# Kernel tuning notes

Measured on AMD Instinct MI355X. Metric: run time of the kernel, lower is better.

Reference implementation:

```python
import jax, jax.numpy as jnp
import numpy as np


def conv3d(x, w, b):
    # x: (B,C,T,W,H), w: (O,I,3,3,3), 'same' padding, stride 1
    y = jax.lax.conv_general_dilated(x, w, (1, 1, 1), [(1, 1)] * 3,
                                     dimension_numbers=('NCDHW', 'OIDHW', 'NCDHW'))
    return y + b[None, :, None, None, None]


def mamba(x, W_in, W_conv, b_conv, W_xproj, W_dt, b_dt, A_log, D, W_out):
    # x: (b, L, d_model) -> (b, L, d_model). Standard Mamba block.
    d_inner, d_state = A_log.shape
    d_conv = W_conv.shape[-1]
    dt_rank = W_dt.shape[1]
    xz = x @ W_in.T                                   # (b, L, 2*d_inner)
    xs, z = jnp.split(xz, 2, axis=-1)
    # causal depthwise conv1d (torch pads d_conv-1 both sides then truncates to L)
    xc = jnp.transpose(xs, (0, 2, 1))                 # (b, d_inner, L)
    xc = jax.lax.conv_general_dilated(xc, W_conv, (1,), [(d_conv - 1, 0)],
                                      feature_group_count=d_inner,
                                      dimension_numbers=('NCH', 'OIH', 'NCH'))
    xc = xc + b_conv[None, :, None]
    xc = jax.nn.silu(jnp.transpose(xc, (0, 2, 1)))    # (b, L, d_inner)
    x_dbl = xc @ W_xproj.T                            # (b, L, dt_rank + 2*d_state)
    dt, B, C = jnp.split(x_dbl, [dt_rank, dt_rank + d_state], axis=-1)
    dt = jax.nn.softplus(dt @ W_dt.T + b_dt)          # (b, L, d_inner)
    A = -jnp.exp(A_log)                               # (d_inner, d_state)
    deltaA = jnp.exp(dt[..., None] * A)               # (b, L, d_inner, d_state)
    deltaBx = dt[..., None] * B[:, :, None, :] * xc[..., None]

    def comb(c1, c2):
        a1, b1 = c1
        a2, b2 = c2
        return a1 * a2, a2 * b1 + b2

    _, hs = jax.lax.associative_scan(comb, (deltaA, deltaBx), axis=1)
    y = jnp.einsum('blds,bls->bld', hs, C) + xc * D   # (b, L, d_inner)
    y = y * jax.nn.silu(z)
    return y @ W_out.T                                # (b, L, d_model)


def setup_inputs() -> dict:
    key = jax.random.key(0)
    ks = jax.random.split(key, 12)
    b, c, t, w, h = 2, 3, 8, 96, 96
    d_state, d_conv, expand = 16, 4, 2
    d_inner = expand * c           # 6
    dt_rank = max(1, -(-c // 16))  # ceil(c/16) = 1

    def n(k, shape, s=0.02):
        return jax.random.normal(k, shape, jnp.float32) * s

    return {
        'x': jax.random.normal(ks[0], (b, c, t, w, h), jnp.float32),
        'W_cb1': n(ks[1], (16, c, 3, 3, 3)), 'b_cb1': jnp.zeros(16, jnp.float32),
        'W_cb2': n(ks[2], (c, 16, 3, 3, 3)), 'b_cb2': jnp.zeros(c, jnp.float32),
        'W_in': n(ks[3], (2 * d_inner, c)),
        'W_conv': n(ks[4], (d_inner, 1, d_conv), 0.2), 'b_conv': jnp.zeros(d_inner, jnp.float32),
        'W_xproj': n(ks[5], (dt_rank + 2 * d_state, d_inner), 0.1),
        'W_dt': n(ks[6], (d_inner, dt_rank), 0.5), 'b_dt': n(ks[7], (d_inner,), 0.1),
        'A_log': jnp.log(jnp.tile(jnp.arange(1, d_state + 1, dtype=jnp.float32)[None, :], (d_inner, 1))),
        'D': jnp.ones(d_inner, jnp.float32),
        'W_out': n(ks[8], (c, d_inner)),
        'W_sm': n(ks[9], (c, c, 3, 3, 3)), 'b_sm': jnp.zeros(c, jnp.float32),
    }


def reference(x, W_cb1, b_cb1, W_cb2, b_cb2, W_in, W_conv, b_conv, W_xproj,
              W_dt, b_dt, A_log, D, W_out, W_sm, b_sm):
    b, c, t, w, h = x.shape
    xr = conv3d(jax.nn.relu(conv3d(x, W_cb1, b_cb1)), W_cb2, b_cb2) + x
    # faithful to torch: x.reshape(b, -1, c) on contiguous (b,c,t,w,h)
    xs = xr.reshape(b, t * w * h, c)
    y = mamba(xs, W_in, W_conv, b_conv, W_xproj, W_dt, b_dt, A_log, D, W_out)
    y = jnp.transpose(y, (0, 2, 1)).reshape(b, c, t, w, h)
    return conv3d(y, W_sm, b_sm)
```

## Files before the change

### kernel.cpp

```cpp
#include <hip/hip_runtime.h>
#include <math.h>

#define L_      73728
#define CTHW_   221184
#define CH_     128
#define NCK_    576
#define STRD_   132
#define LOG2E_  1.4426950408889634f

#define PZS_    9604
#define PCS_    96040
#define XPAD_N  576240
#define T1P_N   3073280
#define YMP_N   576240
#define ZERO_N  (XPAD_N + T1P_N + YMP_N + 16)

__device__ __forceinline__ float silu_(float x) {
    return x / (1.f + __expf(-x));
}
__device__ __forceinline__ float softplus_(float x) {
    return (x > 20.f) ? x : log1pf(__expf(x));
}

__global__ __launch_bounds__(256) void k0_zero(float4* __restrict__ p, int n4) {
    int i = blockIdx.x * 256 + threadIdx.x;
    if (i < n4) p[i] = make_float4(0.f, 0.f, 0.f, 0.f);
}

__global__ __launch_bounds__(256) void k0_copy(const float* __restrict__ x,
        float* __restrict__ xpad) {
    int idx = blockIdx.x * 256 + threadIdx.x;
    int xx = idx % 96, yy = (idx / 96) % 96, z = (idx / 9216) % 8, bc = idx / 73728;
    xpad[bc * PCS_ + (z + 1) * PZS_ + (yy + 1) * 98 + (xx + 1)] = x[idx];
}

__global__ __launch_bounds__(256) void k1_conv(const float* __restrict__ xpad,
        const float* __restrict__ W, const float* __restrict__ b,
        float* __restrict__ t1p) {
    __shared__ float ws[81][16];
    __shared__ float bs[16];
    int tid = threadIdx.x;
    for (int i = tid; i < 1296; i += 256) ws[i % 81][i / 81] = W[i];
    if (tid < 16) bs[tid] = b[tid];
    __syncthreads();
    int idx = blockIdx.x * 256 + tid;
    int xx = idx % 96, yy = (idx / 96) % 96, tz = (idx / 9216) % 8, bb = idx / 73728;
    float acc[16];
    #pragma unroll
    for (int o = 0; o < 16; ++o) acc[o] = bs[o];
    int pbase = (tz + 1) * PZS_ + (yy + 1) * 98 + (xx + 1);
    #pragma unroll
    for (int ic = 0; ic < 3; ++ic) {
        const float* xp = xpad + (bb * 3 + ic) * PCS_ + pbase;
        float v[27];
        #pragma unroll
        for (int kz = 0; kz < 3; ++kz)
            #pragma unroll
            for (int ky = 0; ky < 3; ++ky)
                #pragma unroll
                for (int kx = 0; kx < 3; ++kx)
                    v[kz * 9 + ky * 3 + kx] = xp[(kz - 1) * PZS_ + (ky - 1) * 98 + (kx - 1)];
        #pragma unroll
        for (int k = 0; k < 27; ++k)
            #pragma unroll
            for (int o = 0; o < 16; ++o)
                acc[o] = fmaf(ws[ic * 27 + k][o], v[k], acc[o]);
    }
    float* op = t1p + bb * 16 * PCS_ + pbase;
    #pragma unroll
    for (int o = 0; o < 16; ++o) op[o * PCS_] = fmaxf(acc[o], 0.f);
}

__global__ __launch_bounds__(256) void k2_conv(const float* __restrict__ t1p,
        const float* __restrict__ W, const float* __restrict__ b,
        const float* __restrict__ x, float* __restrict__ xr) {
    __shared__ float ws[432][3];
    __shared__ float bs[3];
    int tid = threadIdx.x;
    for (int i = tid; i < 1296; i += 256) ws[i % 432][i / 432] = W[i];
    if (tid < 3) bs[tid] = b[tid];
    __syncthreads();
    int idx = blockIdx.x * 256 + tid;
    int xx = idx % 96, yy = (idx / 96) % 96, tz = (idx / 9216) % 8, bb = idx / 73728;
    float acc[3];
    #pragma unroll
    for (int o = 0; o < 3; ++o) acc[o] = bs[o];
    int pbase = (tz + 1) * PZS_ + (yy + 1) * 98 + (xx + 1);
    #pragma unroll 2
    for (int ic = 0; ic < 16; ++ic) {
        const float* xp = t1p + (bb * 16 + ic) * PCS_ + pbase;
        float v[27];
        #pragma unroll
        for (int kz = 0; kz < 3; ++kz)
            #pragma unroll
            for (int ky = 0; ky < 3; ++ky)
                #pragma unroll
                for (int kx = 0; kx < 3; ++kx)
                    v[kz * 9 + ky * 3 + kx] = xp[(kz - 1) * PZS_ + (ky - 1) * 98 + (kx - 1)];
        #pragma unroll
        for (int k = 0; k < 27; ++k)
            #pragma unroll
            for (int o = 0; o < 3; ++o)
                acc[o] = fmaf(ws[ic * 27 + k][o], v[k], acc[o]);
    }
    int sp = tz * 9216 + yy * 96 + xx;
    #pragma unroll
    for (int o = 0; o < 3; ++o) {
        int gi = (bb * 3 + o) * 73728 + sp;
        xr[gi] = acc[o] + x[gi];
    }
}

__global__ __launch_bounds__(128) void k4_carry(const float* __restrict__ xr,
        const float* __restrict__ W_in, const float* __restrict__ W_conv,
        const float* __restrict__ b_conv, const float* __restrict__ W_xproj,
        const float* __restrict__ W_dt, const float* __restrict__ b_dt,
        const float* __restrict__ A_log, float2* __restrict__ carries) {
    __shared__ float sf[28 * STRD_];
    __shared__ float s_Win[18], s_Wc[24], s_bc[6], s_Wx[102], s_Wdt[6], s_bdt[6];
    int tid = threadIdx.x;
    if (tid < 18) s_Win[tid] = W_in[tid];
    if (tid < 24) s_Wc[tid] = W_conv[tid];
    if (tid >= 32 && tid < 38) s_bc[tid - 32] = b_conv[tid - 32];
    if (tid >= 40 && tid < 46) { s_Wdt[tid - 40] = W_dt[tid - 40]; s_bdt[tid - 40] = b_dt[tid - 40]; }
    if (tid >= 64 && tid < 128) {
        for (int i = tid - 64; i < 102; i += 64) s_Wx[i] = W_xproj[i];
    }
    __syncthreads();
    int blk = blockIdx.x, b = blk / NCK_, ck = blk % NCK_;
    int l = ck * CH_ + tid;
    const float* xb = xr + b * CTHW_;
    float xin[4][6];
    #pragma unroll
    for (int k = 0; k < 4; ++k) {
        int r = l - 3 + k;
        float a0 = 0.f, a1 = 0.f, a2v = 0.f;
        if (r >= 0) { a0 = xb[3 * r]; a1 = xb[3 * r + 1]; a2v = xb[3 * r + 2]; }
        #pragma unroll
        for (int d = 0; d < 6; ++d)
            xin[k][d] = s_Win[d * 3] * a0 + s_Win[d * 3 + 1] * a1 + s_Win[d * 3 + 2] * a2v;
    }
    float xc[6];
    #pragma unroll
    for (int d = 0; d < 6; ++d) {
        float p = s_bc[d];
        #pragma unroll
        for (int k = 0; k < 4; ++k) p = fmaf(s_Wc[d * 4 + k], xin[k][d], p);
        xc[d] = silu_(p);
    }
    float dtraw = 0.f;
    #pragma unroll
    for (int d = 0; d < 6; ++d) dtraw = fmaf(s_Wx[d], xc[d], dtraw);
    #pragma unroll
    for (int d = 0; d < 6; ++d) {
        sf[(0 + d) * STRD_ + tid] = xc[d];
        sf[(6 + d) * STRD_ + tid] = softplus_(fmaf(dtraw, s_Wdt[d], s_bdt[d]));
    }
    #pragma unroll
    for (int s = 0; s < 16; ++s) {
        float pb = 0.f;
        #pragma unroll
        for (int d = 0; d < 6; ++d) pb = fmaf(s_Wx[(1 + s) * 6 + d], xc[d], pb);
        sf[(12 + s) * STRD_ + tid] = pb;
    }
    __syncthreads();
    if (tid < 96) {
        int d = tid >> 4, s = tid & 15;
        float a2 = -__expf(A_log[tid]) * LOG2E_;
        float h = 0.f, sdt = 0.f;
        #pragma unroll 8
        for (int i = 0; i < CH_; ++i) {
            float dt = sf[(6 + d) * STRD_ + i];
            float xcv = sf[d * STRD_ + i];
            float Bv = sf[(12 + s) * STRD_ + i];
            h = fmaf(exp2f(dt * a2), h, dt * xcv * Bv);
            sdt += dt;
        }
        carries[(b * 96 + tid) * NCK_ + ck] = make_float2(exp2f(sdt * a2), h);
    }
}

__global__ __launch_bounds__(576) void k5_scan(const float2* __restrict__ carries,
        float* __restrict__ hpref) {
    __shared__ float2 s0[NCK_], s1[NCK_];
    int t = threadIdx.x;
    int blk = blockIdx.x, b = blk / 96, r = blk % 96;
    s0[t] = carries[(b * 96 + r) * NCK_ + t];
    __syncthreads();
    float2* cur = s0;
    float2* nxt = s1;
    for (int off = 1; off < NCK_; off <<= 1) {
        float2 v = cur[t];
        if (t >= off) {
            float2 p = cur[t - off];
            v = make_float2(p.x * v.x, v.x * p.y + v.y);
        }
        nxt[t] = v;
        __syncthreads();
        float2* tmp = cur; cur = nxt; nxt = tmp;
    }
    float hp = (t == 0) ? 0.f : cur[t - 1].y;
    hpref[(b * NCK_ + t) * 96 + r] = hp;
}

__global__ __launch_bounds__(128) void k6_apply(const float* __restrict__ xr,
        const float* __restrict__ W_in, const float* __restrict__ W_conv,
        const float* __restrict__ b_conv, const float* __restrict__ W_xproj,
        const float* __restrict__ W_dt, const float* __restrict__ b_dt,
        const float* __restrict__ A_log, const float* __restrict__ Dp,
        const float* __restrict__ W_out, const float* __restrict__ hpref,
        float* __restrict__ ymp) {
    __shared__ float sf[50 * STRD_];
    __shared__ float ys[CH_ * 6];
    __shared__ float s_Win[36], s_Wc[24], s_bc[6], s_Wx[198], s_Wdt[6], s_bdt[6], s_wout[18];
    int tid = threadIdx.x;
    if (tid < 36) s_Win[tid] = W_in[tid];
    if (tid < 24) s_Wc[tid] = W_conv[tid];
    if (tid >= 36 && tid < 42) s_bc[tid - 36] = b_conv[tid - 36];
    if (tid >= 42 && tid < 48) { s_Wdt[tid - 42] = W_dt[tid - 42]; s_bdt[tid - 42] = b_dt[tid - 42]; }
    if (tid >= 48 && tid < 66) s_wout[tid - 48] = W_out[tid - 48];
    if (tid >= 64 && tid < 128) {
        for (int i = tid - 64; i < 198; i += 64) s_Wx[i] = W_xproj[i];
    }
    __syncthreads();
    int blk = blockIdx.x, b = blk / NCK_, ck = blk % NCK_;
    int l = ck * CH_ + tid;
    const float* xb = xr + b * CTHW_;
    float xin[4][6];
    float zv[6];
    #pragma unroll
    for (int k = 0; k < 4; ++k) {
        int r = l - 3 + k;
        float a0 = 0.f, a1 = 0.f, a2v = 0.f;
        if (r >= 0) { a0 = xb[3 * r]; a1 = xb[3 * r + 1]; a2v = xb[3 * r + 2]; }
        #pragma unroll
        for (int d = 0; d < 6; ++d)
            xin[k][d] = s_Win[d * 3] * a0 + s_Win[d * 3 + 1] * a1 + s_Win[d * 3 + 2] * a2v;
        if (k == 3) {
            #pragma unroll
            for (int d = 0; d < 6; ++d)
                zv[d] = s_Win[(6 + d) * 3] * a0 + s_Win[(6 + d) * 3 + 1] * a1 + s_Win[(6 + d) * 3 + 2] * a2v;
        }
    }
    float xc[6];
    #pragma unroll
    for (int d = 0; d < 6; ++d) {
        float p = s_bc[d];
        #pragma unroll
        for (int k = 0; k < 4; ++k) p = fmaf(s_Wc[d * 4 + k], xin[k][d], p);
        xc[d] = silu_(p);
    }
    float dtraw = 0.f;
    #pragma unroll
    for (int d = 0; d < 6; ++d) dtraw = fmaf(s_Wx[d], xc[d], dtraw);
    #pragma unroll
    for (int d = 0; d < 6; ++d) {
        sf[(0 + d) * STRD_ + tid] = xc[d];
        sf[(6 + d) * STRD_ + tid] = softplus_(fmaf(dtraw, s_Wdt[d], s_bdt[d]));
        sf[(12 + d) * STRD_ + tid] = zv[d];
    }
    #pragma unroll
    for (int s = 0; s < 16; ++s) {
        float pb = 0.f, pc = 0.f;
        #pragma unroll
        for (int d = 0; d < 6; ++d) {
            pb = fmaf(s_Wx[(1 + s) * 6 + d], xc[d], pb);
            pc = fmaf(s_Wx[(17 + s) * 6 + d], xc[d], pc);
        }
        sf[(18 + s) * STRD_ + tid] = pb;
        sf[(34 + s) * STRD_ + tid] = pc;
    }
    __syncthreads();
    if (tid < 96) {
        int d = tid >> 4, s = tid & 15;
        float a2 = -__expf(A_log[tid]) * LOG2E_;
        float Dd = Dp[d];
        float h = hpref[(b * NCK_ + ck) * 96 + tid];
        #pragma unroll 4
        for (int i0 = 0; i0 < CH_; i0 += 8) {
            float pb[8], xv[8];
            #pragma unroll
            for (int j = 0; j < 8; ++j) {
                int i = i0 + j;
                float dt = sf[(6 + d) * STRD_ + i];
                float xcv = sf[d * STRD_ + i];
                float Bv = sf[(18 + s) * STRD_ + i];
                float Cv = sf[(34 + s) * STRD_ + i];
                h = fmaf(exp2f(dt * a2), h, dt * xcv * Bv);
                pb[j] = h * Cv;
                xv[j] = xcv;
            }
            #pragma unroll
            for (int j = 0; j < 8; ++j) pb[j] += __shfl_xor(pb[j], 1, 16);
            #pragma unroll
            for (int j = 0; j < 8; ++j) pb[j] += __shfl_xor(pb[j], 2, 16);
            #pragma unroll
            for (int j = 0; j < 8; ++j) pb[j] += __shfl_xor(pb[j], 4, 16);
            #pragma unroll
            for (int j = 0; j < 8; ++j) pb[j] += __shfl_xor(pb[j], 8, 16);
            if (s == 0) {
                #pragma unroll
                for (int j = 0; j < 8; ++j) {
                    float zz = sf[(12 + d) * STRD_ + i0 + j];
                    ys[(i0 + j) * 6 + d] = fmaf(xv[j], Dd, pb[j]) * silu_(zz);
                }
            }
        }
    }
    __syncthreads();
    {
        float y0 = ys[tid * 6 + 0], y1 = ys[tid * 6 + 1], y2 = ys[tid * 6 + 2];
        float y3 = ys[tid * 6 + 3], y4 = ys[tid * 6 + 4], y5 = ys[tid * 6 + 5];
        int xx = l % 96, yy = (l / 96) % 96, tz = l / 9216;
        int pdst = (tz + 1) * PZS_ + (yy + 1) * 98 + (xx + 1);
        #pragma unroll
        for (int i = 0; i < 3; ++i) {
            float o = s_wout[i * 6 + 0] * y0 + s_wout[i * 6 + 1] * y1
                    + s_wout[i * 6 + 2] * y2 + s_wout[i * 6 + 3] * y3
                    + s_wout[i * 6 + 4] * y4 + s_wout[i * 6 + 5] * y5;
            ymp[(b * 3 + i) * PCS_ + pdst] = o;
        }
    }
}

__global__ __launch_bounds__(256) void k7_conv(const float* __restrict__ ymp,
        const float* __restrict__ W, const float* __restrict__ b,
        float* __restrict__ out) {
    __shared__ float ws[81][3];
    __shared__ float bs[3];
    int tid = threadIdx.x;
    for (int i = tid; i < 243; i += 256) ws[i % 81][i / 81] = W[i];
    if (tid < 3) bs[tid] = b[tid];
    __syncthreads();
    int idx = blockIdx.x * 256 + tid;
    int xx = idx % 96, yy = (idx / 96) % 96, tz = (idx / 9216) % 8, bb = idx / 73728;
    float acc[3];
    #pragma unroll
    for (int o = 0; o < 3; ++o) acc[o] = bs[o];
    int pbase = (tz + 1) * PZS_ + (yy + 1) * 98 + (xx + 1);
    #pragma unroll
    for (int ic = 0; ic < 3; ++ic) {
        const float* xp = ymp + (bb * 3 + ic) * PCS_ + pbase;
        float v[27];
        #pragma unroll
        for (int kz = 0; kz < 3; ++kz)
            #pragma unroll
            for (int ky = 0; ky < 3; ++ky)
                #pragma unroll
                for (int kx = 0; kx < 3; ++kx)
                    v[kz * 9 + ky * 3 + kx] = xp[(kz - 1) * PZS_ + (ky - 1) * 98 + (kx - 1)];
        #pragma unroll
        for (int k = 0; k < 27; ++k)
            #pragma unroll
            for (int o = 0; o < 3; ++o)
                acc[o] = fmaf(ws[ic * 27 + k][o], v[k], acc[o]);
    }
    int sp = tz * 9216 + yy * 96 + xx;
    #pragma unroll
    for (int o = 0; o < 3; ++o) out[(bb * 3 + o) * 73728 + sp] = acc[o];
}

extern "C" void kernel_launch(void* const* d_in, const int* in_sizes, int n_in,
                              void* d_out, int out_size, void* d_ws, size_t ws_size,
                              hipStream_t stream) {
    const float* x      = (const float*)d_in[0];
    const float* W_cb1  = (const float*)d_in[1];
    const float* b_cb1  = (const float*)d_in[2];
    const float* W_cb2  = (const float*)d_in[3];
    const float* b_cb2  = (const float*)d_in[4];
    const float* W_in   = (const float*)d_in[5];
    const float* W_conv = (const float*)d_in[6];
    const float* b_conv = (const float*)d_in[7];
    const float* W_xpr  = (const float*)d_in[8];
    const float* W_dt   = (const float*)d_in[9];
    const float* b_dt   = (const float*)d_in[10];
    const float* A_log  = (const float*)d_in[11];
    const float* Dp     = (const float*)d_in[12];
    const float* W_out  = (const float*)d_in[13];
    const float* W_sm   = (const float*)d_in[14];
    const float* b_sm   = (const float*)d_in[15];

    float* ws    = (float*)d_ws;
    float* xpad  = ws;
    float* t1p   = xpad + XPAD_N;
    float* ymp   = t1p + T1P_N;
    float* xr    = ws + ZERO_N;
    float2* carr = (float2*)(xr + 442368);
    float* hpref = xr + 442368 + 221184;
    float* out   = (float*)d_out;

    int n4 = ZERO_N / 4;
    k0_zero<<<(n4 + 255) / 256, 256, 0, stream>>>((float4*)ws, n4);
    k0_copy<<<1728, 256, 0, stream>>>(x, xpad);
    k1_conv<<<576, 256, 0, stream>>>(xpad, W_cb1, b_cb1, t1p);
    k2_conv<<<576, 256, 0, stream>>>(t1p, W_cb2, b_cb2, x, xr);
    k4_carry<<<1152, 128, 0, stream>>>(xr, W_in, W_conv, b_conv, W_xpr, W_dt, b_dt, A_log, carr);
    k5_scan<<<192, 576, 0, stream>>>(carr, hpref);
    k6_apply<<<1152, 128, 0, stream>>>(xr, W_in, W_conv, b_conv, W_xpr, W_dt, b_dt,
                                       A_log, Dp, W_out, hpref, ymp);
    k7_conv<<<576, 256, 0, stream>>>(ymp, W_sm, b_sm, out);
}
```

Before: 195.3 us.

## Register-block conv kernels over 4 outputs and halve scan chunk length

The two 3-output conv kernels now compute four adjacent x-outputs per thread, loading a 6-wide row per kernel row so input loads are reused across outputs. This cuts launched blocks from 576 to 144. The Mamba scan chunk shrinks from 128 to 64 positions, doubling the number of chunks and blocks. k5_scan pre-combines pairs of carries so it can keep 576 threads, then expands the prefix back to per-chunk states. The goal is shorter serial recurrence loops in k4 and k6 at the cost of half-idle threads in the per-position phases, more carry traffic, and fewer blocks for the conv kernels.

After: 214.5 us. 1.1x slower.

```diff
diff --git a/kernel.cpp b/kernel.cpp
--- a/kernel.cpp
+++ b/kernel.cpp
@@ -3,9 +3,9 @@
 
 #define L_      73728
 #define CTHW_   221184
-#define CH_     128
-#define NCK_    576
-#define STRD_   132
+#define CH_     64
+#define NCK_    1152
+#define STRD_   68
 #define LOG2E_  1.4426950408889634f
 
 #define PZS_    9604
@@ -81,34 +81,50 @@
     if (tid < 3) bs[tid] = b[tid];
     __syncthreads();
     int idx = blockIdx.x * 256 + tid;
-    int xx = idx % 96, yy = (idx / 96) % 96, tz = (idx / 9216) % 8, bb = idx / 73728;
-    float acc[3];
-    #pragma unroll
-    for (int o = 0; o < 3; ++o) acc[o] = bs[o];
-    int pbase = (tz + 1) * PZS_ + (yy + 1) * 98 + (xx + 1);
+    int xg = idx % 24, yy = (idx / 24) % 96, tz = (idx / 2304) % 8, bb = idx / 18432;
+    int x0 = xg * 4;
+    float acc[3][4];
+    #pragma unroll
+    for (int o = 0; o < 3; ++o)
+        #pragma unroll
+        for (int u = 0; u < 4; ++u) acc[o][u] = bs[o];
+    int pbase = (tz + 1) * PZS_ + (yy + 1) * 98 + (x0 + 1);
     #pragma unroll 2
     for (int ic = 0; ic < 16; ++ic) {
         const float* xp = t1p + (bb * 16 + ic) * PCS_ + pbase;
-        float v[27];
+        float v[9][6];
         #pragma unroll
         for (int kz = 0; kz < 3; ++kz)
             #pragma unroll
             for (int ky = 0; ky < 3; ++ky)
                 #pragma unroll
-                for (int kx = 0; kx < 3; ++kx)
-                    v[kz * 9 + ky * 3 + kx] = xp[(kz - 1) * PZS_ + (ky - 1) * 98 + (kx - 1)];
-        #pragma unroll
-        for (int k = 0; k < 27; ++k)
-            #pragma unroll
-            for (int o = 0; o < 3; ++o)
-                acc[o] = fmaf(ws[ic * 27 + k][o], v[k], acc[o]);
-    }
-    int sp = tz * 9216 + yy * 96 + xx;
-    #pragma unroll
-    for (int o = 0; o < 3; ++o) {
-        int gi = (bb * 3 + o) * 73728 + sp;
-        xr[gi] = acc[o] + x[gi];
-    }
+                for (int j = 0; j < 6; ++j)
+                    v[kz * 3 + ky][j] = xp[(kz - 1) * PZS_ + (ky - 1) * 98 + (j - 1)];
+        #pragma unroll
+        for (int kz = 0; kz < 3; ++kz)
+            #pragma unroll
+            for (int ky = 0; ky < 3; ++ky)
+                #pragma unroll
+                for (int kx = 0; kx < 3; ++kx) {
+                    int k = ic * 27 + kz * 9 + ky * 3 + kx;
+                    float w0 = ws[k][0], w1 = ws[k][1], w2 = ws[k][2];
+                    #pragma unroll
+                    for (int u = 0; u < 4; ++u) {
+                        float vv = v[kz * 3 + ky][kx + u];
+                        acc[0][u] = fmaf(w0, vv, acc[0][u]);
+                        acc[1][u] = fmaf(w1, vv, acc[1][u]);
+                        acc[2][u] = fmaf(w2, vv, acc[2][u]);
+                    }
+                }
+    }
+    int sp = tz * 9216 + yy * 96 + x0;
+    #pragma unroll
+    for (int o = 0; o < 3; ++o)
+        #pragma unroll
+        for (int u = 0; u < 4; ++u) {
+            int gi = (bb * 3 + o) * 73728 + sp + u;
+            xr[gi] = acc[o][u] + x[gi];
+        }
 }
 
 __global__ __launch_bounds__(128) void k4_carry(const float* __restrict__ xr,
@@ -128,40 +144,42 @@
     }
     __syncthreads();
     int blk = blockIdx.x, b = blk / NCK_, ck = blk % NCK_;
-    int l = ck * CH_ + tid;
-    const float* xb = xr + b * CTHW_;
-    float xin[4][6];
-    #pragma unroll
-    for (int k = 0; k < 4; ++k) {
-        int r = l - 3 + k;
-        float a0 = 0.f, a1 = 0.f, a2v = 0.f;
-        if (r >= 0) { a0 = xb[3 * r]; a1 = xb[3 * r + 1]; a2v = xb[3 * r + 2]; }
-        #pragma unroll
-        for (int d = 0; d < 6; ++d)
-            xin[k][d] = s_Win[d * 3] * a0 + s_Win[d * 3 + 1] * a1 + s_Win[d * 3 + 2] * a2v;
-    }
-    float xc[6];
-    #pragma unroll
-    for (int d = 0; d < 6; ++d) {
-        float p = s_bc[d];
-        #pragma unroll
-        for (int k = 0; k < 4; ++k) p = fmaf(s_Wc[d * 4 + k], xin[k][d], p);
-        xc[d] = silu_(p);
-    }
-    float dtraw = 0.f;
-    #pragma unroll
-    for (int d = 0; d < 6; ++d) dtraw = fmaf(s_Wx[d], xc[d], dtraw);
-    #pragma unroll
-    for (int d = 0; d < 6; ++d) {
-        sf[(0 + d) * STRD_ + tid] = xc[d];
-        sf[(6 + d) * STRD_ + tid] = softplus_(fmaf(dtraw, s_Wdt[d], s_bdt[d]));
-    }
-    #pragma unroll
-    for (int s = 0; s < 16; ++s) {
-        float pb = 0.f;
-        #pragma unroll
-        for (int d = 0; d < 6; ++d) pb = fmaf(s_Wx[(1 + s) * 6 + d], xc[d], pb);
-        sf[(12 + s) * STRD_ + tid] = pb;
+    if (tid < CH_) {
+        int l = ck * CH_ + tid;
+        const float* xb = xr + b * CTHW_;
+        float xin[4][6];
+        #pragma unroll
+        for (int k = 0; k < 4; ++k) {
+            int r = l - 3 + k;
+            float a0 = 0.f, a1 = 0.f, a2v = 0.f;
+            if (r >= 0) { a0 = xb[3 * r]; a1 = xb[3 * r + 1]; a2v = xb[3 * r + 2]; }
+            #pragma unroll
+            for (int d = 0; d < 6; ++d)
+                xin[k][d] = s_Win[d * 3] * a0 + s_Win[d * 3 + 1] * a1 + s_Win[d * 3 + 2] * a2v;
+        }
+        float xc[6];
+        #pragma unroll
+        for (int d = 0; d < 6; ++d) {
+            float p = s_bc[d];
+            #pragma unroll
+            for (int k = 0; k < 4; ++k) p = fmaf(s_Wc[d * 4 + k], xin[k][d], p);
+            xc[d] = silu_(p);
+        }
+        float dtraw = 0.f;
+        #pragma unroll
+        for (int d = 0; d < 6; ++d) dtraw = fmaf(s_Wx[d], xc[d], dtraw);
+        #pragma unroll
+        for (int d = 0; d < 6; ++d) {
+            sf[(0 + d) * STRD_ + tid] = xc[d];
+            sf[(6 + d) * STRD_ + tid] = softplus_(fmaf(dtraw, s_Wdt[d], s_bdt[d]));
+        }
+        #pragma unroll
+        for (int s = 0; s < 16; ++s) {
+            float pb = 0.f;
+            #pragma unroll
+            for (int d = 0; d < 6; ++d) pb = fmaf(s_Wx[(1 + s) * 6 + d], xc[d], pb);
+            sf[(12 + s) * STRD_ + tid] = pb;
+        }
     }
     __syncthreads();
     if (tid < 96) {
@@ -176,20 +194,23 @@
             h = fmaf(exp2f(dt * a2), h, dt * xcv * Bv);
             sdt += dt;
         }
-        carries[(b * 96 + tid) * NCK_ + ck] = make_float2(exp2f(sdt * a2), h);
+        carries[(size_t)(b * 96 + tid) * NCK_ + ck] = make_float2(exp2f(sdt * a2), h);
     }
 }
 
 __global__ __launch_bounds__(576) void k5_scan(const float2* __restrict__ carries,
         float* __restrict__ hpref) {
-    __shared__ float2 s0[NCK_], s1[NCK_];
+    __shared__ float2 s0[576], s1[576];
     int t = threadIdx.x;
     int blk = blockIdx.x, b = blk / 96, r = blk % 96;
-    s0[t] = carries[(b * 96 + r) * NCK_ + t];
+    const float4* cp = (const float4*)(carries + (size_t)(b * 96 + r) * NCK_);
+    float4 cc = cp[t];
+    float2 c0 = make_float2(cc.x, cc.y);
+    s0[t] = make_float2(cc.x * cc.z, cc.z * cc.y + cc.w);
     __syncthreads();
     float2* cur = s0;
     float2* nxt = s1;
-    for (int off = 1; off < NCK_; off <<= 1) {
+    for (int off = 1; off < 576; off <<= 1) {
         float2 v = cur[t];
         if (t >= off) {
             float2 p = cur[t - off];
@@ -199,8 +220,9 @@
         __syncthreads();
         float2* tmp = cur; cur = nxt; nxt = tmp;
     }
-    float hp = (t == 0) ? 0.f : cur[t - 1].y;
-    hpref[(b * NCK_ + t) * 96 + r] = hp;
+    float Ey = (t == 0) ? 0.f : cur[t - 1].y;
+    hpref[(size_t)(b * NCK_ + 2 * t) * 96 + r] = Ey;
+    hpref[(size_t)(b * NCK_ + 2 * t + 1) * 96 + r] = fmaf(c0.x, Ey, c0.y);
 }
 
 __global__ __launch_bounds__(128) void k6_apply(const float* __restrict__ xr,
@@ -211,7 +233,7 @@
         const float* __restrict__ W_out, const float* __restrict__ hpref,
         float* __restrict__ ymp) {
     __shared__ float sf[50 * STRD_];
-    __shared__ float ys[CH_ * 6];
+    __shared__ float ys[CH_ * 7];
     __shared__ float s_Win[36], s_Wc[24], s_bc[6], s_Wx[198], s_Wdt[6], s_bdt[6], s_wout[18];
     int tid = threadIdx.x;
     if (tid < 36) s_Win[tid] = W_in[tid];
@@ -224,59 +246,61 @@
     }
     __syncthreads();
     int blk = blockIdx.x, b = blk / NCK_, ck = blk % NCK_;
-    int l = ck * CH_ + tid;
-    const float* xb = xr + b * CTHW_;
-    float xin[4][6];
-    float zv[6];
-    #pragma unroll
-    for (int k = 0; k < 4; ++k) {
-        int r = l - 3 + k;
-        float a0 = 0.f, a1 = 0.f, a2v = 0.f;
-        if (r >= 0) { a0 = xb[3 * r]; a1 = xb[3 * r + 1]; a2v = xb[3 * r + 2]; }
-        #pragma unroll
-        for (int d = 0; d < 6; ++d)
-            xin[k][d] = s_Win[d * 3] * a0 + s_Win[d * 3 + 1] * a1 + s_Win[d * 3 + 2] * a2v;
-        if (k == 3) {
+    int l = ck * CH_ + (tid & (CH_ - 1));
+    if (tid < CH_) {
+        const float* xb = xr + b * CTHW_;
+        float xin[4][6];
+        float zv[6];
+        #pragma unroll
+        for (int k = 0; k < 4; ++k) {
+            int r = l - 3 + k;
+            float a0 = 0.f, a1 = 0.f, a2v = 0.f;
+            if (r >= 0) { a0 = xb[3 * r]; a1 = xb[3 * r + 1]; a2v = xb[3 * r + 2]; }
             #pragma unroll
             for (int d = 0; d < 6; ++d)
-                zv[d] = s_Win[(6 + d) * 3] * a0 + s_Win[(6 + d) * 3 + 1] * a1 + s_Win[(6 + d) * 3 + 2] * a2v;
-        }
-    }
-    float xc[6];
-    #pragma unroll
-    for (int d = 0; d < 6; ++d) {
-        float p = s_bc[d];
-        #pragma unroll
-        for (int k = 0; k < 4; ++k) p = fmaf(s_Wc[d * 4 + k], xin[k][d], p);
-        xc[d] = silu_(p);
-    }
-    float dtraw = 0.f;
-    #pragma unroll
-    for (int d = 0; d < 6; ++d) dtraw = fmaf(s_Wx[d], xc[d], dtraw);
-    #pragma unroll
-    for (int d = 0; d < 6; ++d) {
-        sf[(0 + d) * STRD_ + tid] = xc[d];
-        sf[(6 + d) * STRD_ + tid] = softplus_(fmaf(dtraw, s_Wdt[d], s_bdt[d]));
-        sf[(12 + d) * STRD_ + tid] = zv[d];
-    }
-    #pragma unroll
-    for (int s = 0; s < 16; ++s) {
-        float pb = 0.f, pc = 0.f;
+                xin[k][d] = s_Win[d * 3] * a0 + s_Win[d * 3 + 1] * a1 + s_Win[d * 3 + 2] * a2v;
+            if (k == 3) {
+                #pragma unroll
+                for (int d = 0; d < 6; ++d)
+                    zv[d] = s_Win[(6 + d) * 3] * a0 + s_Win[(6 + d) * 3 + 1] * a1 + s_Win[(6 + d) * 3 + 2] * a2v;
+            }
+        }
+        float xc[6];
         #pragma unroll
         for (int d = 0; d < 6; ++d) {
-            pb = fmaf(s_Wx[(1 + s) * 6 + d], xc[d], pb);
-            pc = fmaf(s_Wx[(17 + s) * 6 + d], xc[d], pc);
-        }
-        sf[(18 + s) * STRD_ + tid] = pb;
-        sf[(34 + s) * STRD_ + tid] = pc;
+            float p = s_bc[d];
+            #pragma unroll
+            for (int k = 0; k < 4; ++k) p = fmaf(s_Wc[d * 4 + k], xin[k][d], p);
+            xc[d] = silu_(p);
+        }
+        float dtraw = 0.f;
+        #pragma unroll
+        for (int d = 0; d < 6; ++d) dtraw = fmaf(s_Wx[d], xc[d], dtraw);
+        #pragma unroll
+        for (int d = 0; d < 6; ++d) {
+            sf[(0 + d) * STRD_ + tid] = xc[d];
+            sf[(6 + d) * STRD_ + tid] = softplus_(fmaf(dtraw, s_Wdt[d], s_bdt[d]));
+            sf[(12 + d) * STRD_ + tid] = zv[d];
+        }
+        #pragma unroll
+        for (int s = 0; s < 16; ++s) {
+            float pb = 0.f, pc = 0.f;
+            #pragma unroll
+            for (int d = 0; d < 6; ++d) {
+                pb = fmaf(s_Wx[(1 + s) * 6 + d], xc[d], pb);
+                pc = fmaf(s_Wx[(17 + s) * 6 + d], xc[d], pc);
+            }
+            sf[(18 + s) * STRD_ + tid] = pb;
+            sf[(34 + s) * STRD_ + tid] = pc;
+        }
     }
     __syncthreads();
     if (tid < 96) {
         int d = tid >> 4, s = tid & 15;
         float a2 = -__expf(A_log[tid]) * LOG2E_;
         float Dd = Dp[d];
-        float h = hpref[(b * NCK_ + ck) * 96 + tid];
-        #pragma unroll 4
+        float h = hpref[(size_t)(b * NCK_ + ck) * 96 + tid];
+        #pragma unroll 2
         for (int i0 = 0; i0 < CH_; i0 += 8) {
             float pb[8], xv[8];
             #pragma unroll
@@ -302,15 +326,15 @@
                 #pragma unroll
                 for (int j = 0; j < 8; ++j) {
                     float zz = sf[(12 + d) * STRD_ + i0 + j];
-                    ys[(i0 + j) * 6 + d] = fmaf(xv[j], Dd, pb[j]) * silu_(zz);
+                    ys[(i0 + j) * 7 + d] = fmaf(xv[j], Dd, pb[j]) * silu_(zz);
                 }
             }
         }
     }
     __syncthreads();
-    {
-        float y0 = ys[tid * 6 + 0], y1 = ys[tid * 6 + 1], y2 = ys[tid * 6 + 2];
-        float y3 = ys[tid * 6 + 3], y4 = ys[tid * 6 + 4], y5 = ys[tid * 6 + 5];
+    if (tid < CH_) {
+        float y0 = ys[tid * 7 + 0], y1 = ys[tid * 7 + 1], y2 = ys[tid * 7 + 2];
+        float y3 = ys[tid * 7 + 3], y4 = ys[tid * 7 + 4], y5 = ys[tid * 7 + 5];
         int xx = l % 96, yy = (l / 96) % 96, tz = l / 9216;
         int pdst = (tz + 1) * PZS_ + (yy + 1) * 98 + (xx + 1);
         #pragma unroll
@@ -333,31 +357,48 @@
     if (tid < 3) bs[tid] = b[tid];
     __syncthreads();
     int idx = blockIdx.x * 256 + tid;
-    int xx = idx % 96, yy = (idx / 96) % 96, tz = (idx / 9216) % 8, bb = idx / 73728;
-    float acc[3];
-    #pragma unroll
-    for (int o = 0; o < 3; ++o) acc[o] = bs[o];
-    int pbase = (tz + 1) * PZS_ + (yy + 1) * 98 + (xx + 1);
+    int xg = idx % 24, yy = (idx / 24) % 96, tz = (idx / 2304) % 8, bb = idx / 18432;
+    int x0 = xg * 4;
+    float acc[3][4];
+    #pragma unroll
+    for (int o = 0; o < 3; ++o)
+        #pragma unroll
+        for (int u = 0; u < 4; ++u) acc[o][u] = bs[o];
+    int pbase = (tz + 1) * PZS_ + (yy + 1) * 98 + (x0 + 1);
     #pragma unroll
     for (int ic = 0; ic < 3; ++ic) {
         const float* xp = ymp + (bb * 3 + ic) * PCS_ + pbase;
-        float v[27];
+        float v[9][6];
         #pragma unroll
         for (int kz = 0; kz < 3; ++kz)
             #pragma unroll
             for (int ky = 0; ky < 3; ++ky)
                 #pragma unroll
-                for (int kx = 0; kx < 3; ++kx)
-                    v[kz * 9 + ky * 3 + kx] = xp[(kz - 1) * PZS_ + (ky - 1) * 98 + (kx - 1)];
-        #pragma unroll
-        for (int k = 0; k < 27; ++k)
-            #pragma unroll
-            for (int o = 0; o < 3; ++o)
-                acc[o] = fmaf(ws[ic * 27 + k][o], v[k], acc[o]);
-    }
-    int sp = tz * 9216 + yy * 96 + xx;
-    #pragma unroll
-    for (int o = 0; o < 3; ++o) out[(bb * 3 + o) * 73728 + sp] = acc[o];
+                for (int j = 0; j < 6; ++j)
+                    v[kz * 3 + ky][j] = xp[(kz - 1) * PZS_ + (ky - 1) * 98 + (j - 1)];
+        #pragma unroll
+        for (int kz = 0; kz < 3; ++kz)
+            #pragma unroll
+            for (int ky = 0; ky < 3; ++ky)
+                #pragma unroll
+                for (int kx = 0; kx < 3; ++kx) {
+                    int k = ic * 27 + kz * 9 + ky * 3 + kx;
+                    float w0 = ws[k][0], w1 = ws[k][1], w2 = ws[k][2];
+                    #pragma unroll
+                    for (int u = 0; u < 4; ++u) {
+                        float vv = v[kz * 3 + ky][kx + u];
+                        acc[0][u] = fmaf(w0, vv, acc[0][u]);
+                        acc[1][u] = fmaf(w1, vv, acc[1][u]);
+                        acc[2][u] = fmaf(w2, vv, acc[2][u]);
+                    }
+                }
+    }
+    int sp = tz * 9216 + yy * 96 + x0;
+    #pragma unroll
+    for (int o = 0; o < 3; ++o)
+        #pragma unroll
+        for (int u = 0; u < 4; ++u)
+            out[(bb * 3 + o) * 73728 + sp + u] = acc[o][u];
 }
 
 extern "C" void kernel_launch(void* const* d_in, const int* in_sizes, int n_in,
@@ -386,17 +427,17 @@
     float* ymp   = t1p + T1P_N;
     float* xr    = ws + ZERO_N;
     float2* carr = (float2*)(xr + 442368);
-    float* hpref = xr + 442368 + 221184;
+    float* hpref = xr + 442368 + 442368;
     float* out   = (float*)d_out;
 
     int n4 = ZERO_N / 4;
     k0_zero<<<(n4 + 255) / 256, 256, 0, stream>>>((float4*)ws, n4);
     k0_copy<<<1728, 256, 0, stream>>>(x, xpad);
     k1_conv<<<576, 256, 0, stream>>>(xpad, W_cb1, b_cb1, t1p);
-    k2_conv<<<576, 256, 0, stream>>>(t1p, W_cb2, b_cb2, x, xr);
-    k4_carry<<<1152, 128, 0, stream>>>(xr, W_in, W_conv, b_conv, W_xpr, W_dt, b_dt, A_log, carr);
+    k2_conv<<<144, 256, 0, stream>>>(t1p, W_cb2, b_cb2, x, xr);
+    k4_carry<<<2304, 128, 0, stream>>>(xr, W_in, W_conv, b_conv, W_xpr, W_dt, b_dt, A_log, carr);
     k5_scan<<<192, 576, 0, stream>>>(carr, hpref);
-    k6_apply<<<1152, 128, 0, stream>>>(xr, W_in, W_conv, b_conv, W_xpr, W_dt, b_dt,
+    k6_apply<<<2304, 128, 0, stream>>>(xr, W_in, W_conv, b_conv, W_xpr, W_dt, b_dt,
                                        A_log, Dp, W_out, hpref, ymp);
-    k7_conv<<<576, 256, 0, stream>>>(ymp, W_sm, b_sm, out);
-}
+    k7_conv<<<144, 256, 0, stream>>>(ymp, W_sm, b_sm, out);
+}
```

## Halve scan chunk size, pair chunks in scan, swizzle blocks across XCDs

Applied to the files above, without the earlier changes.

Shrinks the selective-scan chunk length to 64, doubling the block count of the carry and apply kernels to expose more parallelism. The scan kernel now combines adjacent chunk pairs while loading so it still runs 576 threads, and it reconstructs the prefix for odd chunks. Block indices of the conv and scan kernels are swizzled in groups of 8 so neighbouring tiles land on the same XCD for L2 locality, and occupancy hints are added to the convs. The ys buffer is padded to stride 7 to avoid LDS bank conflicts. Half the threads now idle during the per-position phase, and writing more carries adds traffic.

After: 191.3 us. 1.02x faster.

```diff
diff --git a/kernel.cpp b/kernel.cpp
--- a/kernel.cpp
+++ b/kernel.cpp
@@ -3,9 +3,9 @@
 
 #define L_      73728
 #define CTHW_   221184
-#define CH_     128
-#define NCK_    576
-#define STRD_   132
+#define CH_     64
+#define NCK_    1152
+#define STRD_   68
 #define LOG2E_  1.4426950408889634f
 
 #define PZS_    9604
@@ -34,7 +34,7 @@
     xpad[bc * PCS_ + (z + 1) * PZS_ + (yy + 1) * 98 + (xx + 1)] = x[idx];
 }
 
-__global__ __launch_bounds__(256) void k1_conv(const float* __restrict__ xpad,
+__global__ __launch_bounds__(256, 4) void k1_conv(const float* __restrict__ xpad,
         const float* __restrict__ W, const float* __restrict__ b,
         float* __restrict__ t1p) {
     __shared__ float ws[81][16];
@@ -43,7 +43,9 @@
     for (int i = tid; i < 1296; i += 256) ws[i % 81][i / 81] = W[i];
     if (tid < 16) bs[tid] = b[tid];
     __syncthreads();
-    int idx = blockIdx.x * 256 + tid;
+    int bid = blockIdx.x;
+    int swz = (bid & 7) * 72 + (bid >> 3);
+    int idx = swz * 256 + tid;
     int xx = idx % 96, yy = (idx / 96) % 96, tz = (idx / 9216) % 8, bb = idx / 73728;
     float acc[16];
     #pragma unroll
@@ -71,7 +73,7 @@
     for (int o = 0; o < 16; ++o) op[o * PCS_] = fmaxf(acc[o], 0.f);
 }
 
-__global__ __launch_bounds__(256) void k2_conv(const float* __restrict__ t1p,
+__global__ __launch_bounds__(256, 4) void k2_conv(const float* __restrict__ t1p,
         const float* __restrict__ W, const float* __restrict__ b,
         const float* __restrict__ x, float* __restrict__ xr) {
     __shared__ float ws[432][3];
@@ -80,7 +82,9 @@
     for (int i = tid; i < 1296; i += 256) ws[i % 432][i / 432] = W[i];
     if (tid < 3) bs[tid] = b[tid];
     __syncthreads();
-    int idx = blockIdx.x * 256 + tid;
+    int bid = blockIdx.x;
+    int swz = (bid & 7) * 72 + (bid >> 3);
+    int idx = swz * 256 + tid;
     int xx = idx % 96, yy = (idx / 96) % 96, tz = (idx / 9216) % 8, bb = idx / 73728;
     float acc[3];
     #pragma unroll
@@ -127,41 +131,45 @@
         for (int i = tid - 64; i < 102; i += 64) s_Wx[i] = W_xproj[i];
     }
     __syncthreads();
-    int blk = blockIdx.x, b = blk / NCK_, ck = blk % NCK_;
-    int l = ck * CH_ + tid;
-    const float* xb = xr + b * CTHW_;
-    float xin[4][6];
-    #pragma unroll
-    for (int k = 0; k < 4; ++k) {
-        int r = l - 3 + k;
-        float a0 = 0.f, a1 = 0.f, a2v = 0.f;
-        if (r >= 0) { a0 = xb[3 * r]; a1 = xb[3 * r + 1]; a2v = xb[3 * r + 2]; }
-        #pragma unroll
-        for (int d = 0; d < 6; ++d)
-            xin[k][d] = s_Win[d * 3] * a0 + s_Win[d * 3 + 1] * a1 + s_Win[d * 3 + 2] * a2v;
-    }
-    float xc[6];
-    #pragma unroll
-    for (int d = 0; d < 6; ++d) {
-        float p = s_bc[d];
-        #pragma unroll
-        for (int k = 0; k < 4; ++k) p = fmaf(s_Wc[d * 4 + k], xin[k][d], p);
-        xc[d] = silu_(p);
-    }
-    float dtraw = 0.f;
-    #pragma unroll
-    for (int d = 0; d < 6; ++d) dtraw = fmaf(s_Wx[d], xc[d], dtraw);
-    #pragma unroll
-    for (int d = 0; d < 6; ++d) {
-        sf[(0 + d) * STRD_ + tid] = xc[d];
-        sf[(6 + d) * STRD_ + tid] = softplus_(fmaf(dtraw, s_Wdt[d], s_bdt[d]));
-    }
-    #pragma unroll
-    for (int s = 0; s < 16; ++s) {
-        float pb = 0.f;
-        #pragma unroll
-        for (int d = 0; d < 6; ++d) pb = fmaf(s_Wx[(1 + s) * 6 + d], xc[d], pb);
-        sf[(12 + s) * STRD_ + tid] = pb;
+    int bid = blockIdx.x;
+    int blk = (bid & 7) * 288 + (bid >> 3);
+    int b = blk / NCK_, ck = blk % NCK_;
+    if (tid < CH_) {
+        int l = ck * CH_ + tid;
+        const float* xb = xr + b * CTHW_;
+        float xin[4][6];
+        #pragma unroll
+        for (int k = 0; k < 4; ++k) {
+            int r = l - 3 + k;
+            float a0 = 0.f, a1 = 0.f, a2v = 0.f;
+            if (r >= 0) { a0 = xb[3 * r]; a1 = xb[3 * r + 1]; a2v = xb[3 * r + 2]; }
+            #pragma unroll
+            for (int d = 0; d < 6; ++d)
+                xin[k][d] = s_Win[d * 3] * a0 + s_Win[d * 3 + 1] * a1 + s_Win[d * 3 + 2] * a2v;
+        }
+        float xc[6];
+        #pragma unroll
+        for (int d = 0; d < 6; ++d) {
+            float p = s_bc[d];
+            #pragma unroll
+            for (int k = 0; k < 4; ++k) p = fmaf(s_Wc[d * 4 + k], xin[k][d], p);
+            xc[d] = silu_(p);
+        }
+        float dtraw = 0.f;
+        #pragma unroll
+        for (int d = 0; d < 6; ++d) dtraw = fmaf(s_Wx[d], xc[d], dtraw);
+        #pragma unroll
+        for (int d = 0; d < 6; ++d) {
+            sf[(0 + d) * STRD_ + tid] = xc[d];
+            sf[(6 + d) * STRD_ + tid] = softplus_(fmaf(dtraw, s_Wdt[d], s_bdt[d]));
+        }
+        #pragma unroll
+        for (int s = 0; s < 16; ++s) {
+            float pb = 0.f;
+            #pragma unroll
+            for (int d = 0; d < 6; ++d) pb = fmaf(s_Wx[(1 + s) * 6 + d], xc[d], pb);
+            sf[(12 + s) * STRD_ + tid] = pb;
+        }
     }
     __syncthreads();
     if (tid < 96) {
@@ -176,20 +184,23 @@
             h = fmaf(exp2f(dt * a2), h, dt * xcv * Bv);
             sdt += dt;
         }
-        carries[(b * 96 + tid) * NCK_ + ck] = make_float2(exp2f(sdt * a2), h);
+        carries[(size_t)(b * 96 + tid) * NCK_ + ck] = make_float2(exp2f(sdt * a2), h);
     }
 }
 
 __global__ __launch_bounds__(576) void k5_scan(const float2* __restrict__ carries,
         float* __restrict__ hpref) {
-    __shared__ float2 s0[NCK_], s1[NCK_];
+    __shared__ float2 s0[576], s1[576];
     int t = threadIdx.x;
     int blk = blockIdx.x, b = blk / 96, r = blk % 96;
-    s0[t] = carries[(b * 96 + r) * NCK_ + t];
+    const float4* cp = (const float4*)(carries + (size_t)(b * 96 + r) * NCK_);
+    float4 cc = cp[t];
+    float2 c0 = make_float2(cc.x, cc.y);
+    s0[t] = make_float2(cc.x * cc.z, cc.z * cc.y + cc.w);
     __syncthreads();
     float2* cur = s0;
     float2* nxt = s1;
-    for (int off = 1; off < NCK_; off <<= 1) {
+    for (int off = 1; off < 576; off <<= 1) {
         float2 v = cur[t];
         if (t >= off) {
             float2 p = cur[t - off];
@@ -199,8 +210,9 @@
         __syncthreads();
         float2* tmp = cur; cur = nxt; nxt = tmp;
     }
-    float hp = (t == 0) ? 0.f : cur[t - 1].y;
-    hpref[(b * NCK_ + t) * 96 + r] = hp;
+    float Ey = (t == 0) ? 0.f : cur[t - 1].y;
+    hpref[(size_t)(b * NCK_ + 2 * t) * 96 + r] = Ey;
+    hpref[(size_t)(b * NCK_ + 2 * t + 1) * 96 + r] = fmaf(c0.x, Ey, c0.y);
 }
 
 __global__ __launch_bounds__(128) void k6_apply(const float* __restrict__ xr,
@@ -211,7 +223,7 @@
         const float* __restrict__ W_out, const float* __restrict__ hpref,
         float* __restrict__ ymp) {
     __shared__ float sf[50 * STRD_];
-    __shared__ float ys[CH_ * 6];
+    __shared__ float ys[CH_ * 7];
     __shared__ float s_Win[36], s_Wc[24], s_bc[6], s_Wx[198], s_Wdt[6], s_bdt[6], s_wout[18];
     int tid = threadIdx.x;
     if (tid < 36) s_Win[tid] = W_in[tid];
@@ -223,60 +235,64 @@
         for (int i = tid - 64; i < 198; i += 64) s_Wx[i] = W_xproj[i];
     }
     __syncthreads();
-    int blk = blockIdx.x, b = blk / NCK_, ck = blk % NCK_;
-    int l = ck * CH_ + tid;
-    const float* xb = xr + b * CTHW_;
-    float xin[4][6];
-    float zv[6];
-    #pragma unroll
-    for (int k = 0; k < 4; ++k) {
-        int r = l - 3 + k;
-        float a0 = 0.f, a1 = 0.f, a2v = 0.f;
-        if (r >= 0) { a0 = xb[3 * r]; a1 = xb[3 * r + 1]; a2v = xb[3 * r + 2]; }
-        #pragma unroll
-        for (int d = 0; d < 6; ++d)
-            xin[k][d] = s_Win[d * 3] * a0 + s_Win[d * 3 + 1] * a1 + s_Win[d * 3 + 2] * a2v;
-        if (k == 3) {
+    int bid = blockIdx.x;
+    int blk = (bid & 7) * 288 + (bid >> 3);
+    int b = blk / NCK_, ck = blk % NCK_;
+    int l = ck * CH_ + (tid & (CH_ - 1));
+    if (tid < CH_) {
+        const float* xb = xr + b * CTHW_;
+        float xin[4][6];
+        float zv[6];
+        #pragma unroll
+        for (int k = 0; k < 4; ++k) {
+            int r = l - 3 + k;
+            float a0 = 0.f, a1 = 0.f, a2v = 0.f;
+            if (r >= 0) { a0 = xb[3 * r]; a1 = xb[3 * r + 1]; a2v = xb[3 * r + 2]; }
             #pragma unroll
             for (int d = 0; d < 6; ++d)
-                zv[d] = s_Win[(6 + d) * 3] * a0 + s_Win[(6 + d) * 3 + 1] * a1 + s_Win[(6 + d) * 3 + 2] * a2v;
-        }
-    }
-    float xc[6];
-    #pragma unroll
-    for (int d = 0; d < 6; ++d) {
-        float p = s_bc[d];
-        #pragma unroll
-        for (int k = 0; k < 4; ++k) p = fmaf(s_Wc[d * 4 + k], xin[k][d], p);
-        xc[d] = silu_(p);
-    }
-    float dtraw = 0.f;
-    #pragma unroll
-    for (int d = 0; d < 6; ++d) dtraw = fmaf(s_Wx[d], xc[d], dtraw);
-    #pragma unroll
-    for (int d = 0; d < 6; ++d) {
-        sf[(0 + d) * STRD_ + tid] = xc[d];
-        sf[(6 + d) * STRD_ + tid] = softplus_(fmaf(dtraw, s_Wdt[d], s_bdt[d]));
-        sf[(12 + d) * STRD_ + tid] = zv[d];
-    }
-    #pragma unroll
-    for (int s = 0; s < 16; ++s) {
-        float pb = 0.f, pc = 0.f;
+                xin[k][d] = s_Win[d * 3] * a0 + s_Win[d * 3 + 1] * a1 + s_Win[d * 3 + 2] * a2v;
+            if (k == 3) {
+                #pragma unroll
+                for (int d = 0; d < 6; ++d)
+                    zv[d] = s_Win[(6 + d) * 3] * a0 + s_Win[(6 + d) * 3 + 1] * a1 + s_Win[(6 + d) * 3 + 2] * a2v;
+            }
+        }
+        float xc[6];
         #pragma unroll
         for (int d = 0; d < 6; ++d) {
-            pb = fmaf(s_Wx[(1 + s) * 6 + d], xc[d], pb);
-            pc = fmaf(s_Wx[(17 + s) * 6 + d], xc[d], pc);
-        }
-        sf[(18 + s) * STRD_ + tid] = pb;
-        sf[(34 + s) * STRD_ + tid] = pc;
+            float p = s_bc[d];
+            #pragma unroll
+            for (int k = 0; k < 4; ++k) p = fmaf(s_Wc[d * 4 + k], xin[k][d], p);
+            xc[d] = silu_(p);
+        }
+        float dtraw = 0.f;
+        #pragma unroll
+        for (int d = 0; d < 6; ++d) dtraw = fmaf(s_Wx[d], xc[d], dtraw);
+        #pragma unroll
+        for (int d = 0; d < 6; ++d) {
+            sf[(0 + d) * STRD_ + tid] = xc[d];
+            sf[(6 + d) * STRD_ + tid] = softplus_(fmaf(dtraw, s_Wdt[d], s_bdt[d]));
+            sf[(12 + d) * STRD_ + tid] = zv[d];
+        }
+        #pragma unroll
+        for (int s = 0; s < 16; ++s) {
+            float pb = 0.f, pc = 0.f;
+            #pragma unroll
+            for (int d = 0; d < 6; ++d) {
+                pb = fmaf(s_Wx[(1 + s) * 6 + d], xc[d], pb);
+                pc = fmaf(s_Wx[(17 + s) * 6 + d], xc[d], pc);
+            }
+            sf[(18 + s) * STRD_ + tid] = pb;
+            sf[(34 + s) * STRD_ + tid] = pc;
+        }
     }
     __syncthreads();
     if (tid < 96) {
         int d = tid >> 4, s = tid & 15;
         float a2 = -__expf(A_log[tid]) * LOG2E_;
         float Dd = Dp[d];
-        float h = hpref[(b * NCK_ + ck) * 96 + tid];
-        #pragma unroll 4
+        float h = hpref[(size_t)(b * NCK_ + ck) * 96 + tid];
+        #pragma unroll 2
         for (int i0 = 0; i0 < CH_; i0 += 8) {
             float pb[8], xv[8];
             #pragma unroll
@@ -302,15 +318,15 @@
                 #pragma unroll
                 for (int j = 0; j < 8; ++j) {
                     float zz = sf[(12 + d) * STRD_ + i0 + j];
-                    ys[(i0 + j) * 6 + d] = fmaf(xv[j], Dd, pb[j]) * silu_(zz);
+                    ys[(i0 + j) * 7 + d] = fmaf(xv[j], Dd, pb[j]) * silu_(zz);
                 }
             }
         }
     }
     __syncthreads();
-    {
-        float y0 = ys[tid * 6 + 0], y1 = ys[tid * 6 + 1], y2 = ys[tid * 6 + 2];
-        float y3 = ys[tid * 6 + 3], y4 = ys[tid * 6 + 4], y5 = ys[tid * 6 + 5];
+    if (tid < CH_) {
+        float y0 = ys[tid * 7 + 0], y1 = ys[tid * 7 + 1], y2 = ys[tid * 7 + 2];
+        float y3 = ys[tid * 7 + 3], y4 = ys[tid * 7 + 4], y5 = ys[tid * 7 + 5];
         int xx = l % 96, yy = (l / 96) % 96, tz = l / 9216;
         int pdst = (tz + 1) * PZS_ + (yy + 1) * 98 + (xx + 1);
         #pragma unroll
@@ -323,7 +339,7 @@
     }
 }
 
-__global__ __launch_bounds__(256) void k7_conv(const float* __restrict__ ymp,
+__global__ __launch_bounds__(256, 4) void k7_conv(const float* __restrict__ ymp,
         const float* __restrict__ W, const float* __restrict__ b,
         float* __restrict__ out) {
     __shared__ float ws[81][3];
@@ -332,7 +348,9 @@
     for (int i = tid; i < 243; i += 256) ws[i % 81][i / 81] = W[i];
     if (tid < 3) bs[tid] = b[tid];
     __syncthreads();
-    int idx = blockIdx.x * 256 + tid;
+    int bid = blockIdx.x;
+    int swz = (bid & 7) * 72 + (bid >> 3);
+    int idx = swz * 256 + tid;
     int xx = idx % 96, yy = (idx / 96) % 96, tz = (idx / 9216) % 8, bb = idx / 73728;
     float acc[3];
     #pragma unroll
@@ -386,7 +404,7 @@
     float* ymp   = t1p + T1P_N;
     float* xr    = ws + ZERO_N;
     float2* carr = (float2*)(xr + 442368);
-    float* hpref = xr + 442368 + 221184;
+    float* hpref = xr + 442368 + 442368;
     float* out   = (float*)d_out;
 
     int n4 = ZERO_N / 4;
@@ -394,9 +412,9 @@
     k0_copy<<<1728, 256, 0, stream>>>(x, xpad);
     k1_conv<<<576, 256, 0, stream>>>(xpad, W_cb1, b_cb1, t1p);
     k2_conv<<<576, 256, 0, stream>>>(t1p, W_cb2, b_cb2, x, xr);
-    k4_carry<<<1152, 128, 0, stream>>>(xr, W_in, W_conv, b_conv, W_xpr, W_dt, b_dt, A_log, carr);
+    k4_carry<<<2304, 128, 0, stream>>>(xr, W_in, W_conv, b_conv, W_xpr, W_dt, b_dt, A_log, carr);
     k5_scan<<<192, 576, 0, stream>>>(carr, hpref);
-    k6_apply<<<1152, 128, 0, stream>>>(xr, W_in, W_conv, b_conv, W_xpr, W_dt, b_dt,
+    k6_apply<<<2304, 128, 0, stream>>>(xr, W_in, W_conv, b_conv, W_xpr, W_dt, b_dt,
                                        A_log, Dp, W_out, hpref, ymp);
     k7_conv<<<576, 256, 0, stream>>>(ymp, W_sm, b_sm, out);
 }
```
